# Kernel optimization log

Hardware: AMD Instinct MI355X
Metric: run time of the kernel (lower is better)

The kernel has to match this reference:

```python
import jax, jax.numpy as jnp
import numpy as np

D_MODEL = 512
N_HEADS = 8
HEAD_DIM = D_MODEL // N_HEADS
BATCH = 4
SEQ = 2048


def setup_inputs() -> dict:
    key = jax.random.key(0)
    ks = jax.random.split(key, 9)
    s = 1.0 / np.sqrt(D_MODEL)
    inp = {
        "x": jax.random.normal(ks[0], (BATCH, SEQ, D_MODEL), dtype=jnp.float32),
        "wq": jax.random.uniform(ks[1], (D_MODEL, D_MODEL), jnp.float32, -s, s),
        "bq": jax.random.uniform(ks[2], (D_MODEL,), jnp.float32, -s, s),
        "wk": jax.random.uniform(ks[3], (D_MODEL, D_MODEL), jnp.float32, -s, s),
        "bk": jax.random.uniform(ks[4], (D_MODEL,), jnp.float32, -s, s),
        "wv": jax.random.uniform(ks[5], (D_MODEL, D_MODEL), jnp.float32, -s, s),
        "bv": jax.random.uniform(ks[6], (D_MODEL,), jnp.float32, -s, s),
        "wo": jax.random.uniform(ks[7], (D_MODEL, D_MODEL), jnp.float32, -s, s),
        "bo": jax.random.uniform(ks[8], (D_MODEL,), jnp.float32, -s, s),
    }
    return inp


def reference(x, wq, bq, wk, bk, wv, bv, wo, bo):
    B, S, D = x.shape
    H, Hd = N_HEADS, HEAD_DIM
    # projections (torch Linear: y = x @ W^T + b; here weights stored as [in, out])
    q = (x @ wq + bq).reshape(B, S, H, Hd).transpose(0, 2, 1, 3)  # [B,H,S,Hd]
    k = (x @ wk + bk).reshape(B, S, H, Hd).transpose(0, 2, 1, 3)
    v = (x @ wv + bv).reshape(B, S, H, Hd).transpose(0, 2, 1, 3)
    scores = jnp.einsum("bhqd,bhkd->bhqk", q, k) / jnp.sqrt(jnp.float32(Hd))
    attn = jax.nn.softmax(scores, axis=-1)
    o = jnp.einsum("bhqk,bhkd->bhqd", attn, v)  # [B,H,S,Hd]
    o = o.transpose(0, 2, 1, 3).reshape(B, S, D)
    return o @ wo + bo
```

## Files before the change

### kernel.cpp

```cpp
#include <hip/hip_runtime.h>
#include <math.h>

#define DM   512
#define SEQL 2048
#define NB   4
#define NH   8
#define HD   64

typedef _Float16 f16;
typedef __fp16   fp16x2 __attribute__((ext_vector_type(2)));
typedef _Float16 f16x4 __attribute__((ext_vector_type(4)));
typedef _Float16 f16x8 __attribute__((ext_vector_type(8)));
typedef float    f32x4 __attribute__((ext_vector_type(4)));
typedef unsigned int u32x2 __attribute__((ext_vector_type(2)));

#define QSCALE 0.1803368801f
#define SOFTMAX_SHIFT 4.328085123f

typedef const __attribute__((address_space(1))) void* gp1_t;
typedef __attribute__((address_space(3))) void* lp3_t;
__device__ __forceinline__ void glds16(const void* g, void* l) {
    __builtin_amdgcn_global_load_lds((gp1_t)g, (lp3_t)l, 16, 0, 0);
}

__device__ __forceinline__ float fast_exp2(float x) {
    return __builtin_amdgcn_exp2f(x);
}

__global__ __launch_bounds__(256) void prep_kernel(
    const float* __restrict__ x, f16* __restrict__ xh,
    const float* __restrict__ w0, const float* __restrict__ w1,
    const float* __restrict__ w2, const float* __restrict__ w3,
    f16* __restrict__ o0, f16* __restrict__ o1,
    f16* __restrict__ o2, f16* __restrict__ o3)
{
    __shared__ f16 t[64][72];
    const int bx = blockIdx.x;
    if (bx < 2048) {
        int i = (bx * 256 + threadIdx.x) * 8;
        float4 a = *(const float4*)&x[i];
        float4 b = *(const float4*)&x[i + 4];
        f16x8 h;
        h[0] = (f16)a.x; h[1] = (f16)a.y; h[2] = (f16)a.z; h[3] = (f16)a.w;
        h[4] = (f16)b.x; h[5] = (f16)b.y; h[6] = (f16)b.z; h[7] = (f16)b.w;
        *(f16x8*)&xh[i] = h;
        return;
    }
    const int idx  = bx - 2048;
    const int wsel = idx >> 6, tile = idx & 63;
    const float* w; f16* o;
    switch (wsel) {
        case 0:  w = w0; o = o0; break;
        case 1:  w = w1; o = o1; break;
        case 2:  w = w2; o = o2; break;
        default: w = w3; o = o3; break;
    }
    const int n0 = (tile & 7) * 64, k0 = (tile >> 3) * 64;
    const int tx = threadIdx.x & 63, tg = threadIdx.x >> 6;
    #pragma unroll
    for (int r = 0; r < 16; ++r) {
        int kl = tg * 16 + r;
        t[tx][kl] = (f16)w[(size_t)(k0 + kl) * DM + n0 + tx];
    }
    __syncthreads();
    #pragma unroll
    for (int r = 0; r < 16; ++r) {
        int nl = tg * 16 + r;
        o[(size_t)(n0 + nl) * DM + k0 + tx] = t[nl][tx];
    }
}

__global__ __launch_bounds__(256) void gemm_qkv(
    const f16* __restrict__ A, const f16* __restrict__ Wt,
    const float* __restrict__ bq, const float* __restrict__ bk,
    const float* __restrict__ bv,
    f16* __restrict__ qh, f16* __restrict__ kh, f16* __restrict__ vth)
{
    __shared__ __align__(16) char smem[34816];
    f16* As_ = (f16*)smem;
    f16* Bs_ = (f16*)(smem + 16384);
    f16* T   = (f16*)smem;

    const int tid  = threadIdx.x;
    const int lane = tid & 63, wave = tid >> 6;
    const int quad = lane >> 4, l15 = lane & 15;
    const int wm = wave >> 1, wn = wave & 1;

    const int bid = blockIdx.x;
    const int r8  = bid & 7;
    const int tt  = bid >> 3;
    const int j   = tt % 12;
    const int mm  = tt / 12;
    const int n0  = j * 128;
    const int m0  = (mm * 8 + r8) * 128;
    const bool qk = (j < 8);

    const int sr16 = lane >> 2;
    const int sk   = (lane & 3) * 8;

    auto stage = [&](int k0, int buf) {
        #pragma unroll
        for (int rb = 0; rb < 2; ++rb) {
            const int row = wave * 32 + rb * 16;
            glds16(&A [(size_t)(m0 + row + sr16) * DM + k0 + sk],
                   &As_[buf * 4096 + row * 32]);
            glds16(&Wt[(size_t)(n0 + row + sr16) * DM + k0 + sk],
                   &Bs_[buf * 4096 + row * 32]);
        }
    };

    f32x4 acc[4][4] = {};
    stage(0, 0);

    for (int it = 0; it < 16; ++it) {
        __syncthreads();
        if (it < 15) stage((it + 1) * 32, (it + 1) & 1);
        const int buf = (it & 1) * 4096;

        f16x8 af[4], bf[4];
        #pragma unroll
        for (int i = 0; i < 4; ++i)
            af[i] = *(f16x8*)&As_[buf + (wm * 64 + i * 16 + l15) * 32 + quad * 8];
        #pragma unroll
        for (int i = 0; i < 4; ++i)
            bf[i] = *(f16x8*)&Bs_[buf + (wn * 64 + i * 16 + l15) * 32 + quad * 8];
        if (qk) {
            #pragma unroll
            for (int i = 0; i < 4; ++i)
                #pragma unroll
                for (int jj = 0; jj < 4; ++jj)
                    acc[i][jj] = __builtin_amdgcn_mfma_f32_16x16x32_f16(
                        bf[i], af[jj], acc[i][jj], 0, 0, 0);
        } else {
            #pragma unroll
            for (int i = 0; i < 4; ++i)
                #pragma unroll
                for (int jj = 0; jj < 4; ++jj)
                    acc[i][jj] = __builtin_amdgcn_mfma_f32_16x16x32_f16(
                        af[i], bf[jj], acc[i][jj], 0, 0, 0);
        }
    }
    __syncthreads();

    const int seg  = n0 >> 9;
    const int nn0b = n0 & 511;
    const int b    = m0 >> 11, s0 = m0 & 2047;

    if (qk) {
        const float* bp = seg == 0 ? bq : bk;
        #pragma unroll
        for (int i = 0; i < 4; ++i) {
            const int nb = wn * 64 + i * 16 + quad * 4;
            f32x4 bv4 = *(const f32x4*)&bp[nn0b + nb];
            #pragma unroll
            for (int jj = 0; jj < 4; ++jj) {
                const int ml = wm * 64 + jj * 16 + l15;
                f16x4 pk;
                #pragma unroll
                for (int rr = 0; rr < 4; ++rr) pk[rr] = (f16)(acc[i][jj][rr] + bv4[rr]);
                *(f16x4*)&T[ml * 136 + nb] = pk;
            }
        }
        __syncthreads();
        f16* op = seg == 0 ? qh : kh;
        #pragma unroll
        for (int r = 0; r < 8; ++r) {
            const int idx = r * 256 + tid;
            const int ml = idx >> 4, c = (idx & 15) * 8;
            f16x8 v = *(f16x8*)&T[ml * 136 + c];
            const int nn = nn0b + c;
            const int hh = nn >> 6, hd8 = nn & 63;
            *(f16x8*)&op[(((size_t)(b * NH + hh) * SEQL + s0 + ml) << 6) + hd8] = v;
        }
    } else {
        #pragma unroll
        for (int jj = 0; jj < 4; ++jj) {
            const int nl = wn * 64 + jj * 16 + l15;
            const float bias = bv[nn0b + nl];
            #pragma unroll
            for (int i = 0; i < 4; ++i) {
                const int mb = wm * 64 + i * 16 + quad * 4;
                f16x4 pk;
                #pragma unroll
                for (int rr = 0; rr < 4; ++rr) pk[rr] = (f16)(acc[i][jj][rr] + bias);
                *(f16x4*)&T[nl * 136 + mb] = pk;
            }
        }
        __syncthreads();
        #pragma unroll
        for (int r = 0; r < 8; ++r) {
            const int idx = r * 256 + tid;
            const int nl = idx >> 4, c = (idx & 15) * 8;
            f16x8 v = *(f16x8*)&T[nl * 136 + c];
            const int nn = nn0b + nl;
            const int hh = nn >> 6, hd = nn & 63;
            *(f16x8*)&vth[(((size_t)(b * NH + hh) * HD + hd) << 11) + s0 + c] = v;
        }
    }
}

__global__ __launch_bounds__(256) void gemm_out(
    const f16* __restrict__ A, const f16* __restrict__ Wt,
    const float* __restrict__ bias, float* __restrict__ out)
{
    __shared__ __align__(16) char smem[67584];
    f16*   As_ = (f16*)smem;
    f16*   Bs_ = (f16*)(smem + 16384);
    float* T3  = (float*)smem;

    const int tid  = threadIdx.x;
    const int lane = tid & 63, wave = tid >> 6;
    const int quad = lane >> 4, l15 = lane & 15;
    const int wm = wave >> 1, wn = wave & 1;
    const int n0 = blockIdx.x * 128, m0 = blockIdx.y * 128;

    const int sr16 = lane >> 2;
    const int sk   = (lane & 3) * 8;

    auto stage = [&](int k0, int buf) {
        #pragma unroll
        for (int rb = 0; rb < 2; ++rb) {
            const int row = wave * 32 + rb * 16;
            glds16(&A [(size_t)(m0 + row + sr16) * DM + k0 + sk],
                   &As_[buf * 4096 + row * 32]);
            glds16(&Wt[(size_t)(n0 + row + sr16) * DM + k0 + sk],
                   &Bs_[buf * 4096 + row * 32]);
        }
    };

    f32x4 acc[4][4] = {};
    stage(0, 0);

    for (int it = 0; it < 16; ++it) {
        __syncthreads();
        if (it < 15) stage((it + 1) * 32, (it + 1) & 1);
        const int buf = (it & 1) * 4096;

        f16x8 af[4], bf[4];
        #pragma unroll
        for (int i = 0; i < 4; ++i)
            af[i] = *(f16x8*)&As_[buf + (wm * 64 + i * 16 + l15) * 32 + quad * 8];
        #pragma unroll
        for (int i = 0; i < 4; ++i)
            bf[i] = *(f16x8*)&Bs_[buf + (wn * 64 + i * 16 + l15) * 32 + quad * 8];
        #pragma unroll
        for (int i = 0; i < 4; ++i)
            #pragma unroll
            for (int jj = 0; jj < 4; ++jj)
                acc[i][jj] = __builtin_amdgcn_mfma_f32_16x16x32_f16(
                    bf[i], af[jj], acc[i][jj], 0, 0, 0);
    }
    __syncthreads();

    #pragma unroll
    for (int i = 0; i < 4; ++i) {
        const int nb = wn * 64 + i * 16 + quad * 4;
        f32x4 bv4 = *(const f32x4*)&bias[n0 + nb];
        #pragma unroll
        for (int jj = 0; jj < 4; ++jj) {
            const int ml = wm * 64 + jj * 16 + l15;
            *(f32x4*)&T3[ml * 132 + nb] = acc[i][jj] + bv4;
        }
    }
    __syncthreads();
    #pragma unroll
    for (int r = 0; r < 16; ++r) {
        const int idx = r * 256 + tid;
        const int ml = idx >> 5, c = (idx & 31) * 4;
        f32x4 v = *(f32x4*)&T3[ml * 132 + c];
        *(f32x4*)&out[(size_t)(m0 + ml) * DM + n0 + c] = v;
    }
}

__global__ __launch_bounds__(512) void flash_attn_mfma(
    const f16* __restrict__ Q, const f16* __restrict__ K,
    const f16* __restrict__ Vt, f16* __restrict__ O)
{
    __shared__ __align__(16) char smem[35840];
    f16*   Ks = (f16*)smem;
    f16*   Vs = (f16*)(smem + 16384);
    float* cs = (float*)smem;
    float* Lx = (float*)(smem + 34816);

    const int tid  = threadIdx.x;
    const int lane = tid & 63, wave = tid >> 6;
    const int quad = lane >> 4, l15 = lane & 15;
    const int g  = wave >> 2;
    const int qg = wave & 3;
    const int x7 = l15 & 7;

    const int id = blockIdx.x;
    const int r8 = id & 7;
    const int tt = id >> 3;
    const int j  = tt & 15;
    const int bh = (tt >> 4) * 8 + r8;
    const int q0 = j * 128;
    const int b = bh >> 3, h = bh & 7;

    const f16* Qb = Q  + (size_t)bh * SEQL * HD;
    const f16* Kb = K  + (size_t)bh * SEQL * HD;
    const f16* Vb = Vt + (size_t)bh * HD * SEQL;

    f16x8 qf[2][2];
    #pragma unroll
    for (int mq = 0; mq < 2; ++mq)
        #pragma unroll
        for (int ks = 0; ks < 2; ++ks) {
            qf[mq][ks] = *(const f16x8*)
                &Qb[(size_t)(q0 + qg * 32 + mq * 16 + l15) * HD + ks * 32 + quad * 8];
            #pragma unroll
            for (int jj = 0; jj < 8; ++jj) qf[mq][ks][jj] *= (f16)QSCALE;
        }

    f16x8 onesf;
    #pragma unroll
    for (int jj = 0; jj < 8; ++jj) onesf[jj] = (f16)1.0f;

    const int krow = tid >> 3;
    const int ku   = tid & 7;
    const int vrow = tid >> 4;
    const int vu   = tid & 15;
    const int kch  = ku * 8, vch = vu * 8;

    f16x8 kreg[2], vreg[2];
    #pragma unroll
    for (int r = 0; r < 2; ++r) {
        kreg[r] = *(const f16x8*)&Kb[(size_t)(krow + r * 64) * HD + kch];
        vreg[r] = *(const f16x8*)&Vb[(size_t)(vrow + r * 32) * SEQL + vch];
    }

    f32x4 o_acc[2][4] = {};
    f32x4 o_l[2] = {};

    for (int kt = 0; kt < SEQL / 128; ++kt) {
        __syncthreads();
        #pragma unroll
        for (int r = 0; r < 2; ++r) {
            const int krw = krow + r * 64;
            const int vrw = vrow + r * 32;
            *(f16x8*)&Ks[krw * 64  + ((ku ^ (krow & 7)) << 3)] = kreg[r];
            *(f16x8*)&Vs[vrw * 128 + ((vu ^ (vrow & 7)) << 3)] = vreg[r];
        }
        __syncthreads();
        if (kt < SEQL / 128 - 1) {
            const int kb2 = (kt + 1) * 128;
            #pragma unroll
            for (int r = 0; r < 2; ++r) {
                kreg[r] = *(const f16x8*)&Kb[(size_t)(kb2 + krow + r * 64) * HD + kch];
                vreg[r] = *(const f16x8*)&Vb[(size_t)(vrow + r * 32) * SEQL + kb2 + vch];
            }
        }

        f32x4 sc[4][2];
        #pragma unroll
        for (int mk = 0; mk < 4; ++mk)
            #pragma unroll
            for (int mq = 0; mq < 2; ++mq)
                sc[mk][mq] = (f32x4){-SOFTMAX_SHIFT, -SOFTMAX_SHIFT,
                                     -SOFTMAX_SHIFT, -SOFTMAX_SHIFT};
        #pragma unroll
        for (int ks = 0; ks < 2; ++ks) {
            #pragma unroll
            for (int mk = 0; mk < 4; ++mk) {
                f16x8 af = *(f16x8*)&Ks[(g * 64 + mk * 16 + l15) * 64
                                        + (((ks * 4 + quad) ^ x7) << 3)];
                #pragma unroll
                for (int mq = 0; mq < 2; ++mq)
                    sc[mk][mq] = __builtin_amdgcn_mfma_f32_16x16x32_f16(
                        af, qf[mq][ks], sc[mk][mq], 0, 0, 0);
            }
        }

        f16x8 pa[2][2];
        #pragma unroll
        for (int kc = 0; kc < 2; ++kc)
            #pragma unroll
            for (int mq = 0; mq < 2; ++mq) {
                const f32x4 sA = sc[kc * 2][mq];
                const f32x4 sB = sc[kc * 2 + 1][mq];
                union { unsigned u; fp16x2 h; } wA0, wA1, wB0, wB1;
                wA0.h = __builtin_amdgcn_cvt_pkrtz(fast_exp2(sA[0]), fast_exp2(sA[1]));
                wA1.h = __builtin_amdgcn_cvt_pkrtz(fast_exp2(sA[2]), fast_exp2(sA[3]));
                wB0.h = __builtin_amdgcn_cvt_pkrtz(fast_exp2(sB[0]), fast_exp2(sB[1]));
                wB1.h = __builtin_amdgcn_cvt_pkrtz(fast_exp2(sB[2]), fast_exp2(sB[3]));
                u32x2 r0 = __builtin_amdgcn_permlane32_swap(wA0.u, wB0.u, false, false);
                u32x2 r1 = __builtin_amdgcn_permlane16_swap(r0[0], r0[1], false, false);
                u32x2 r2 = __builtin_amdgcn_permlane32_swap(wA1.u, wB1.u, false, false);
                u32x2 r3 = __builtin_amdgcn_permlane16_swap(r2[0], r2[1], false, false);
                union { f16x8 v; unsigned u[4]; } P;
                P.u[0] = r1[0];
                P.u[1] = r3[0];
                P.u[2] = r1[1];
                P.u[3] = r3[1];
                pa[kc][mq] = P.v;
            }

        #pragma unroll
        for (int kc = 0; kc < 2; ++kc) {
            o_l[0] = __builtin_amdgcn_mfma_f32_16x16x32_f16(pa[kc][0], onesf, o_l[0], 0, 0, 0);
            o_l[1] = __builtin_amdgcn_mfma_f32_16x16x32_f16(pa[kc][1], onesf, o_l[1], 0, 0, 0);
            #pragma unroll
            for (int nt = 0; nt < 4; ++nt) {
                f16x8 vb = *(f16x8*)&Vs[(nt * 16 + l15) * 128
                                        + (((g * 8 + kc * 4 + quad) ^ x7) << 3)];
                o_acc[0][nt] = __builtin_amdgcn_mfma_f32_16x16x32_f16(
                    pa[kc][0], vb, o_acc[0][nt], 0, 0, 0);
                o_acc[1][nt] = __builtin_amdgcn_mfma_f32_16x16x32_f16(
                    pa[kc][1], vb, o_acc[1][nt], 0, 0, 0);
            }
        }
    }

    __syncthreads();
    if (l15 == 0) {
        #pragma unroll
        for (int mq = 0; mq < 2; ++mq)
            #pragma unroll
            for (int r = 0; r < 4; ++r)
                Lx[wave * 32 + mq * 16 + quad * 4 + r] = o_l[mq][r];
    }
    if (g == 1) {
        #pragma unroll
        for (int mq = 0; mq < 2; ++mq)
            #pragma unroll
            for (int r = 0; r < 4; ++r) {
                const int ql = mq * 16 + quad * 4 + r;
                #pragma unroll
                for (int nt = 0; nt < 4; ++nt)
                    cs[(qg * 32 + ql) * 68 + nt * 16 + l15] = o_acc[mq][nt][r];
            }
    }
    __syncthreads();
    if (g == 0) {
        #pragma unroll
        for (int mq = 0; mq < 2; ++mq)
            #pragma unroll
            for (int r = 0; r < 4; ++r) {
                const int ql = mq * 16 + quad * 4 + r;
                const float inv = 1.0f / (Lx[qg * 32 + ql] + Lx[(4 + qg) * 32 + ql]);
                const int s = q0 + qg * 32 + ql;
                #pragma unroll
                for (int nt = 0; nt < 4; ++nt) {
                    float ov = o_acc[mq][nt][r] + cs[(qg * 32 + ql) * 68 + nt * 16 + l15];
                    O[((size_t)(b * SEQL + s)) * DM + h * HD + nt * 16 + l15] =
                        (f16)(ov * inv);
                }
            }
    }
}

extern "C" void kernel_launch(void* const* d_in, const int* in_sizes, int n_in,
                              void* d_out, int out_size, void* d_ws, size_t ws_size,
                              hipStream_t stream) {
    const float* x  = (const float*)d_in[0];
    const float* wq = (const float*)d_in[1];
    const float* bq = (const float*)d_in[2];
    const float* wk = (const float*)d_in[3];
    const float* bk = (const float*)d_in[4];
    const float* wv = (const float*)d_in[5];
    const float* bv = (const float*)d_in[6];
    const float* wo = (const float*)d_in[7];
    const float* bo = (const float*)d_in[8];

    const size_t NE = (size_t)NB * SEQL * DM;
    const size_t WE = (size_t)DM * DM;
    f16* xh    = (f16*)d_ws;
    f16* wqkvt = xh + NE;
    f16* wot   = wqkvt + 3 * WE;
    f16* qh    = wot + WE;
    f16* kh    = qh + NE;
    f16* vth   = kh + NE;
    f16* oh    = vth + NE;

    prep_kernel<<<2304, 256, 0, stream>>>(
        x, xh, wq, wk, wv, wo,
        wqkvt, wqkvt + WE, wqkvt + 2 * WE, wot);

    gemm_qkv<<<768, 256, 0, stream>>>(
        xh, wqkvt, bq, bk, bv, qh, kh, vth);

    flash_attn_mfma<<<512, 512, 0, stream>>>(qh, kh, vth, oh);

    gemm_out<<<dim3(4, 64), 256, 0, stream>>>(oh, wot, bo, (float*)d_out);
}
```

Before: 154.7 us.

## Double-buffer K/V tiles in LDS via direct global-to-LDS async loads

Replaces the register-staged K/V prefetch in the flash attention kernel with direct global_load_lds transfers into a double-buffered LDS region, swizzling on the global address side. Each iteration issues the next tile's loads into the alternate buffer, then computes on the current one, with a single barrier per iteration instead of two. This is meant to cut VGPR pressure and LDS write instructions and to overlap loads with MFMA work. The cost is LDS use rising to 64KB per block, which may lower occupancy.

```diff
diff --git a/kernel.cpp b/kernel.cpp
--- a/kernel.cpp
+++ b/kernel.cpp
@@ -276,9 +276,7 @@
     const f16* __restrict__ Q, const f16* __restrict__ K,
     const f16* __restrict__ Vt, f16* __restrict__ O)
 {
-    __shared__ __align__(16) char smem[35840];
-    f16*   Ks = (f16*)smem;
-    f16*   Vs = (f16*)(smem + 16384);
+    __shared__ __align__(16) char smem[65536];
     float* cs = (float*)smem;
     float* Lx = (float*)(smem + 34816);
 
@@ -316,40 +314,34 @@
     #pragma unroll
     for (int jj = 0; jj < 8; ++jj) onesf[jj] = (f16)1.0f;
 
-    const int krow = tid >> 3;
-    const int ku   = tid & 7;
-    const int vrow = tid >> 4;
-    const int vu   = tid & 15;
-    const int kch  = ku * 8, vch = vu * 8;
-
-    f16x8 kreg[2], vreg[2];
-    #pragma unroll
-    for (int r = 0; r < 2; ++r) {
-        kreg[r] = *(const f16x8*)&Kb[(size_t)(krow + r * 64) * HD + kch];
-        vreg[r] = *(const f16x8*)&Vb[(size_t)(vrow + r * 32) * SEQL + vch];
-    }
+    const int kl3 = lane >> 3, ku8 = lane & 7;
+    const int vl4 = lane >> 4, vu16 = lane & 15;
+
+    auto stage = [&](int kb, int buf) {
+        char* base = smem + buf * 32768;
+        #pragma unroll
+        for (int r = 0; r < 2; ++r) {
+            const int blk = wave + r * 8;
+            const int kr  = blk * 8 + kl3;
+            glds16(&Kb[(size_t)(kb + kr) * HD + ((ku8 ^ (kr & 7)) << 3)],
+                   base + blk * 1024);
+            const int vr  = blk * 4 + vl4;
+            glds16(&Vb[(size_t)vr * SEQL + kb + ((vu16 ^ (vr & 7)) << 3)],
+                   base + 16384 + blk * 1024);
+        }
+    };
 
     f32x4 o_acc[2][4] = {};
     f32x4 o_l[2] = {};
 
+    stage(0, 0);
+    __syncthreads();
+
+    int cur = 0;
     for (int kt = 0; kt < SEQL / 128; ++kt) {
-        __syncthreads();
-        #pragma unroll
-        for (int r = 0; r < 2; ++r) {
-            const int krw = krow + r * 64;
-            const int vrw = vrow + r * 32;
-            *(f16x8*)&Ks[krw * 64  + ((ku ^ (krow & 7)) << 3)] = kreg[r];
-            *(f16x8*)&Vs[vrw * 128 + ((vu ^ (vrow & 7)) << 3)] = vreg[r];
-        }
-        __syncthreads();
-        if (kt < SEQL / 128 - 1) {
-            const int kb2 = (kt + 1) * 128;
-            #pragma unroll
-            for (int r = 0; r < 2; ++r) {
-                kreg[r] = *(const f16x8*)&Kb[(size_t)(kb2 + krow + r * 64) * HD + kch];
-                vreg[r] = *(const f16x8*)&Vb[(size_t)(vrow + r * 32) * SEQL + kb2 + vch];
-            }
-        }
+        if (kt < SEQL / 128 - 1) stage((kt + 1) * 128, cur ^ 1);
+        const f16* Ks = (const f16*)(smem + cur * 32768);
+        const f16* Vs = (const f16*)(smem + cur * 32768 + 16384);
 
         f32x4 sc[4][2];
         #pragma unroll
@@ -362,8 +354,8 @@
         for (int ks = 0; ks < 2; ++ks) {
             #pragma unroll
             for (int mk = 0; mk < 4; ++mk) {
-                f16x8 af = *(f16x8*)&Ks[(g * 64 + mk * 16 + l15) * 64
-                                        + (((ks * 4 + quad) ^ x7) << 3)];
+                f16x8 af = *(const f16x8*)&Ks[(g * 64 + mk * 16 + l15) * 64
+                                              + (((ks * 4 + quad) ^ x7) << 3)];
                 #pragma unroll
                 for (int mq = 0; mq < 2; ++mq)
                     sc[mk][mq] = __builtin_amdgcn_mfma_f32_16x16x32_f16(
@@ -401,17 +393,19 @@
             o_l[1] = __builtin_amdgcn_mfma_f32_16x16x32_f16(pa[kc][1], onesf, o_l[1], 0, 0, 0);
             #pragma unroll
             for (int nt = 0; nt < 4; ++nt) {
-                f16x8 vb = *(f16x8*)&Vs[(nt * 16 + l15) * 128
-                                        + (((g * 8 + kc * 4 + quad) ^ x7) << 3)];
+                f16x8 vb = *(const f16x8*)&Vs[(nt * 16 + l15) * 128
+                                              + (((g * 8 + kc * 4 + quad) ^ x7) << 3)];
                 o_acc[0][nt] = __builtin_amdgcn_mfma_f32_16x16x32_f16(
                     pa[kc][0], vb, o_acc[0][nt], 0, 0, 0);
                 o_acc[1][nt] = __builtin_amdgcn_mfma_f32_16x16x32_f16(
                     pa[kc][1], vb, o_acc[1][nt], 0, 0, 0);
             }
         }
-    }
-
-    __syncthreads();
+
+        __syncthreads();
+        cur ^= 1;
+    }
+
     if (l15 == 0) {
         #pragma unroll
         for (int mq = 0; mq < 2; ++mq)
```

Result: no change. 157.5 us (+1.8%).

## Fuse fp32-to-fp16 conversion of x into QKV GEMM operand loading

Applied to the files above, without the earlier changes.

Drops the separate conversion pass that wrote an fp16 copy of x. The QKV GEMM now loads fp32 x through registers two k-steps ahead, converts it to fp16, and writes it into LDS, while the weight tiles still use direct global-to-LDS loads. This removes one write and one read of the x-sized intermediate and shrinks the prep kernel. In exchange, each GEMM block reads x as fp32 (twice the bytes, and repeated across the 12 N-tiles) and holds extra registers for the prefetch.

```diff
diff --git a/kernel.cpp b/kernel.cpp
--- a/kernel.cpp
+++ b/kernel.cpp
@@ -28,25 +28,13 @@
 }
 
 __global__ __launch_bounds__(256) void prep_kernel(
-    const float* __restrict__ x, f16* __restrict__ xh,
     const float* __restrict__ w0, const float* __restrict__ w1,
     const float* __restrict__ w2, const float* __restrict__ w3,
     f16* __restrict__ o0, f16* __restrict__ o1,
     f16* __restrict__ o2, f16* __restrict__ o3)
 {
     __shared__ f16 t[64][72];
-    const int bx = blockIdx.x;
-    if (bx < 2048) {
-        int i = (bx * 256 + threadIdx.x) * 8;
-        float4 a = *(const float4*)&x[i];
-        float4 b = *(const float4*)&x[i + 4];
-        f16x8 h;
-        h[0] = (f16)a.x; h[1] = (f16)a.y; h[2] = (f16)a.z; h[3] = (f16)a.w;
-        h[4] = (f16)b.x; h[5] = (f16)b.y; h[6] = (f16)b.z; h[7] = (f16)b.w;
-        *(f16x8*)&xh[i] = h;
-        return;
-    }
-    const int idx  = bx - 2048;
+    const int idx  = blockIdx.x;
     const int wsel = idx >> 6, tile = idx & 63;
     const float* w; f16* o;
     switch (wsel) {
@@ -71,7 +59,7 @@
 }
 
 __global__ __launch_bounds__(256) void gemm_qkv(
-    const f16* __restrict__ A, const f16* __restrict__ Wt,
+    const float* __restrict__ X, const f16* __restrict__ Wt,
     const float* __restrict__ bq, const float* __restrict__ bk,
     const float* __restrict__ bv,
     f16* __restrict__ qh, f16* __restrict__ kh, f16* __restrict__ vth)
@@ -98,24 +86,52 @@
     const int sr16 = lane >> 2;
     const int sk   = (lane & 3) * 8;
 
-    auto stage = [&](int k0, int buf) {
+    auto stageB = [&](int k0, int buf) {
         #pragma unroll
         for (int rb = 0; rb < 2; ++rb) {
             const int row = wave * 32 + rb * 16;
-            glds16(&A [(size_t)(m0 + row + sr16) * DM + k0 + sk],
-                   &As_[buf * 4096 + row * 32]);
             glds16(&Wt[(size_t)(n0 + row + sr16) * DM + k0 + sk],
                    &Bs_[buf * 4096 + row * 32]);
         }
     };
 
+    const int arow = tid >> 2;
+    const int akq  = (tid & 3) * 8;
+    float4 a0[2], a1[2];
+    auto ldA = [&](int k0) {
+        #pragma unroll
+        for (int r = 0; r < 2; ++r) {
+            const float* p = &X[(size_t)(m0 + r * 64 + arow) * DM + k0 + akq];
+            a0[r] = *(const float4*)p;
+            a1[r] = *(const float4*)(p + 4);
+        }
+    };
+    auto stA = [&](int buf) {
+        #pragma unroll
+        for (int r = 0; r < 2; ++r) {
+            f16x8 h;
+            h[0] = (f16)a0[r].x; h[1] = (f16)a0[r].y;
+            h[2] = (f16)a0[r].z; h[3] = (f16)a0[r].w;
+            h[4] = (f16)a1[r].x; h[5] = (f16)a1[r].y;
+            h[6] = (f16)a1[r].z; h[7] = (f16)a1[r].w;
+            *(f16x8*)&As_[buf * 4096 + r * 2048 + tid * 8] = h;
+        }
+    };
+
     f32x4 acc[4][4] = {};
-    stage(0, 0);
+    ldA(0);
+    stageB(0, 0);
+    stA(0);
+    ldA(32);
 
     for (int it = 0; it < 16; ++it) {
         __syncthreads();
-        if (it < 15) stage((it + 1) * 32, (it + 1) & 1);
         const int buf = (it & 1) * 4096;
+        if (it < 15) {
+            stageB((it + 1) * 32, (it + 1) & 1);
+            stA((it + 1) & 1);
+        }
+        if (it < 14) ldA((it + 2) * 32);
 
         f16x8 af[4], bf[4];
         #pragma unroll
@@ -464,20 +480,19 @@
 
     const size_t NE = (size_t)NB * SEQL * DM;
     const size_t WE = (size_t)DM * DM;
-    f16* xh    = (f16*)d_ws;
-    f16* wqkvt = xh + NE;
+    f16* wqkvt = (f16*)d_ws;
     f16* wot   = wqkvt + 3 * WE;
     f16* qh    = wot + WE;
     f16* kh    = qh + NE;
     f16* vth   = kh + NE;
     f16* oh    = vth + NE;
 
-    prep_kernel<<<2304, 256, 0, stream>>>(
-        x, xh, wq, wk, wv, wo,
+    prep_kernel<<<256, 256, 0, stream>>>(
+        wq, wk, wv, wo,
         wqkvt, wqkvt + WE, wqkvt + 2 * WE, wot);
 
     gemm_qkv<<<768, 256, 0, stream>>>(
-        xh, wqkvt, bq, bk, bv, qh, kh, vth);
+        x, wqkvt, bq, bk, bv, qh, kh, vth);
 
     flash_attn_mfma<<<512, 512, 0, stream>>>(qh, kh, vth, oh);
 
```

Result: slower. 159.1 us (+2.9%).
